# Kernel optimization log

Hardware: AMD Instinct MI355X
Metric: run time of the kernel (lower is better)

The kernel has to match this reference:

```python
import jax, jax.numpy as jnp
import numpy as np

B, N, C, S, G, COOR = 4, 8192, 64, 2048, 32, 3
C2 = 2 * C            # channels after SetAbstraction
EXP = 4
RADII = (0.2, 0.4, 0.4)


def _sqdist(src, dst):
    # (B,M,3),(B,N,3) -> (B,M,N) squared distances (same expansion as torch code)
    d = -2.0 * jnp.einsum('bmc,bnc->bmn', src, dst)
    d = d + jnp.sum(src ** 2, -1)[:, :, None]
    d = d + jnp.sum(dst ** 2, -1)[:, None, :]
    return d


def _gather(points, idx):
    # points (B,N,C), idx (B,...) -> (B,...,C)
    return jax.vmap(lambda p, i: p[i])(points, idx)


def _fps(xyz, npoint):
    # xyz (B,N,3) -> (B,npoint) farthest point sample indices (start at index 0)
    b, n, _ = xyz.shape

    def step(carry, _):
        distance, farthest = carry
        centroid = jnp.take_along_axis(xyz, farthest[:, None, None], axis=1)  # (B,1,3)
        d = jnp.sqrt(jnp.sum((xyz - centroid) ** 2, -1))
        distance = jnp.minimum(distance, d)
        nxt = jnp.argmax(distance, -1)
        return (distance, nxt), farthest

    init = (jnp.full((b, n), 1e10, xyz.dtype), jnp.zeros((b,), jnp.int32))
    _, idxs = jax.lax.scan(step, init, None, length=npoint)
    return jnp.transpose(idxs)  # (B,npoint)


def _query_hybrid(radius, nsample, xyz, new_xyz):
    d = _sqdist(new_xyz, xyz)                       # (B,S,N)
    neg_d, idx = jax.lax.top_k(-d, nsample)         # smallest distances
    mask = (-neg_d) > radius ** 2
    first = idx[:, :, :1]
    return jnp.where(mask, first, idx)              # (B,S,nsample)


def _group(coor, new_coor, fea, radius, nsample):
    # coor (B,N,3), new_coor (B,S,3), fea (B,N,C) -> (B,S,G,C+3)
    gi = _query_hybrid(radius, nsample, coor, new_coor)
    gc = (_gather(coor, gi) - new_coor[:, :, None, :]) / radius
    gf = _gather(fea, gi)
    return jnp.concatenate([gf, gc], axis=-1)


def _mlp_max(g, w):
    # g (B,S,G,Cin), w (Cout,Cin): 1x1 conv (no bias) + ReLU, then max over group
    h = jax.nn.relu(jnp.einsum('bsgc,dc->bsgd', g, w))
    return jnp.max(h, axis=2)  # (B,S,Cout)


def _inv_res_mlp(coor, fea, radius, nsample, w_la, w1, w2):
    # coor (B,S,3), fea (B,S,C2) channels-last
    identity = fea
    g = _group(coor, coor, fea, radius, nsample)
    fea = _mlp_max(g, w_la)                              # LocalAggregation
    fea = jax.nn.relu(jnp.einsum('bsc,dc->bsd', fea, w1))
    fea = jnp.einsum('bsc,dc->bsd', fea, w2)             # last ReLU dropped
    return jax.nn.relu(fea + identity)


def setup_inputs() -> dict:
    key = jax.random.key(0)
    ks = jax.random.split(key, 10)
    def w(k, o, i):
        return jax.random.normal(k, (o, i), jnp.float32) / np.sqrt(i)
    return {
        'points_coor': jax.random.uniform(ks[0], (B, 3, N), jnp.float32),
        'points_fea': jax.random.normal(ks[1], (B, C, N), jnp.float32),
        'w_sa':  w(ks[2], C2, C + COOR),
        'w_la1': w(ks[3], C2, C2 + COOR),
        'w1_1':  w(ks[4], C2 * EXP, C2),
        'w2_1':  w(ks[5], C2, C2 * EXP),
        'w_la2': w(ks[6], C2, C2 + COOR),
        'w1_2':  w(ks[7], C2 * EXP, C2),
        'w2_2':  w(ks[8], C2, C2 * EXP),
    }


def reference(points_coor, points_fea, w_sa, w_la1, w1_1, w2_1, w_la2, w1_2, w2_2):
    coor = jnp.transpose(points_coor, (0, 2, 1))  # (B,N,3)
    fea = jnp.transpose(points_fea, (0, 2, 1))    # (B,N,C)
    # SetAbstraction: S-G-P
    fps_idx = _fps(coor, S)
    new_coor = _gather(coor, fps_idx)             # (B,S,3)
    g = _group(coor, new_coor, fea, RADII[0], G)
    new_fea = _mlp_max(g, w_sa)                   # (B,S,2C)
    # InvResMLP blocks
    new_fea = _inv_res_mlp(new_coor, new_fea, RADII[1], G, w_la1, w1_1, w2_1)
    new_fea = _inv_res_mlp(new_coor, new_fea, RADII[2], G, w_la2, w1_2, w2_2)
    return (jnp.transpose(new_coor, (0, 2, 1)), jnp.transpose(new_fea, (0, 2, 1)))
```

## Files before the change

### kernel.cpp

```cpp
#include <hip/hip_runtime.h>
#include <hip/hip_bf16.h>

#define BB 4
#define NN 8192
#define CC 64
#define SS 2048
#define GG 32
#define C2V 128
#define HHV 512

typedef unsigned long long u64;
typedef unsigned int u32;

__global__ void k_transpose_fea(const float* __restrict__ in, float* __restrict__ out) {
  __shared__ float tile[32][33];
  const int b = blockIdx.z;
  const int n0 = blockIdx.x * 32, c0 = blockIdx.y * 32;
  const int tx = threadIdx.x, ty = threadIdx.y;
  const float* src = in + (size_t)b * CC * NN;
#pragma unroll
  for (int i = 0; i < 32; i += 8)
    tile[ty + i][tx] = src[(size_t)(c0 + ty + i) * NN + n0 + tx];
  __syncthreads();
  float* dst = out + (size_t)b * NN * CC;
#pragma unroll
  for (int i = 0; i < 32; i += 8)
    dst[(size_t)(n0 + ty + i) * CC + c0 + tx] = tile[tx][ty + i];
}

__global__ __launch_bounds__(1024, 4) void k_fps(const float* __restrict__ pc, int* __restrict__ fps_idx) {
#pragma clang fp contract(off)
  __shared__ float lx[NN], ly[NN], lz[NN];
  __shared__ int sIdx[SS];
  __shared__ u64 sK[2][16];
  const int b = blockIdx.x, tid = threadIdx.x;
  const int lane = tid & 63, wid = tid >> 6;
  const float* pb = pc + (size_t)b * 3 * NN;
  {
    const float4* gx = (const float4*)pb;
    const float4* gy = (const float4*)(pb + NN);
    const float4* gz = (const float4*)(pb + 2 * NN);
    float4* sx = (float4*)lx; float4* sy = (float4*)ly; float4* sz = (float4*)lz;
    sx[tid] = gx[tid]; sx[tid + 1024] = gx[tid + 1024];
    sy[tid] = gy[tid]; sy[tid + 1024] = gy[tid + 1024];
    sz[tid] = gz[tid]; sz[tid + 1024] = gz[tid + 1024];
  }
  if (tid < 32) ((u64*)sK)[tid] = 0ull;
  if (tid == 0) sK[0][0] = ~0ull;
  __syncthreads();

  const int fbase = wid * 64 + lane;
  const u32 ibase = (u32)(wid * 256 + lane * 4);
  float4 D0 = make_float4(1e20f, 1e20f, 1e20f, 1e20f);
  float4 D1 = D0;

#define DPPK64(K, CTL) { \
      u32 lo = (u32)(K), hi = (u32)((K) >> 32); \
      u32 lo2 = (u32)__builtin_amdgcn_update_dpp(0, (int)lo, CTL, 0xf, 0xf, false); \
      u32 hi2 = (u32)__builtin_amdgcn_update_dpp(0, (int)hi, CTL, 0xf, 0xf, false); \
      u64 k2 = ((u64)hi2 << 32) | (u64)lo2; if (k2 > (K)) (K) = k2; }
#define RMAXF(V, CTL) { \
      float t_ = __int_as_float(__builtin_amdgcn_update_dpp(0, __float_as_int(V), CTL, 0xf, 0xf, false)); \
      (V) = fmaxf((V), t_); }
#define RMINU(V, CTL) { \
      u32 t_ = (u32)__builtin_amdgcn_update_dpp(0, (int)(V), CTL, 0xf, 0xf, false); \
      (V) = min((V), t_); }

  for (int k = 0; k < SS; ++k) {
    const int p = k & 1, pn = p ^ 1;
    u64 kk = sK[p][lane & 15];
    const float4 Xa = ((const float4*)lx)[fbase], Xb = ((const float4*)lx)[fbase + 1024];
    const float4 Ya = ((const float4*)ly)[fbase], Yb = ((const float4*)ly)[fbase + 1024];
    const float4 Za = ((const float4*)lz)[fbase], Zb = ((const float4*)lz)[fbase + 1024];
    DPPK64(kk, 0x121) DPPK64(kk, 0x122) DPPK64(kk, 0x124) DPPK64(kk, 0x128)
    const u32 idx = 0xFFFFFFFFu - (u32)kk;
    if (tid == 0) sIdx[k] = (int)idx;
    const float cx = lx[idx], cy = ly[idx], cz = lz[idx];

#define UPDC(XX, YY, ZZ, DD) { \
      float dx_ = (XX) - cx, dy_ = (YY) - cy, dz_ = (ZZ) - cz; \
      float t0_ = dx_ * dx_, t1_ = dy_ * dy_, t2_ = dz_ * dz_; \
      float s_ = (t0_ + t1_) + t2_; \
      (DD) = fminf((DD), s_); }
    UPDC(Xa.x, Ya.x, Za.x, D0.x) UPDC(Xa.y, Ya.y, Za.y, D0.y)
    UPDC(Xa.z, Ya.z, Za.z, D0.z) UPDC(Xa.w, Ya.w, Za.w, D0.w)
    UPDC(Xb.x, Yb.x, Zb.x, D1.x) UPDC(Xb.y, Yb.y, Zb.y, D1.y)
    UPDC(Xb.z, Yb.z, Zb.z, D1.z) UPDC(Xb.w, Yb.w, Zb.w, D1.w)
#undef UPDC

    float m2 = fmaxf(fmaxf(fmaxf(D0.x, D0.y), fmaxf(D0.z, D0.w)),
                     fmaxf(fmaxf(D1.x, D1.y), fmaxf(D1.z, D1.w)));
    RMAXF(m2, 0x121) RMAXF(m2, 0x122) RMAXF(m2, 0x124) RMAXF(m2, 0x128)
    m2 = fmaxf(m2, __shfl_xor(m2, 16, 64));
    m2 = fmaxf(m2, __shfl_xor(m2, 32, 64));

    float s = sqrtf(m2);
    u32 sbits = __float_as_uint(s);
    float spred = __uint_as_float(sbits - 1u);
    double M = ((double)spred + (double)s) * 0.5;
    double L = M * M;
    if (sbits & 1u) L = __longlong_as_double(__double_as_longlong(L) + 1ll);
    float Lf = (float)L;
    if ((double)Lf < L) Lf = __uint_as_float(__float_as_uint(Lf) + 1u);

    u32 enc = 0xFFFFFFFFu;
    {
      int off = -1;
      if (D1.w >= Lf) off = 4096 + 3;
      if (D1.z >= Lf) off = 4096 + 2;
      if (D1.y >= Lf) off = 4096 + 1;
      if (D1.x >= Lf) off = 4096 + 0;
      if (D0.w >= Lf) off = 3;
      if (D0.z >= Lf) off = 2;
      if (D0.y >= Lf) off = 1;
      if (D0.x >= Lf) off = 0;
      if (off >= 0) enc = ibase + (u32)off;
    }
    RMINU(enc, 0x121) RMINU(enc, 0x122) RMINU(enc, 0x124) RMINU(enc, 0x128)
    enc = min(enc, (u32)__shfl_xor((int)enc, 16, 64));
    enc = min(enc, (u32)__shfl_xor((int)enc, 32, 64));

    if (lane == 0)
      sK[pn][wid] = (((u64)sbits) << 32) | (u64)(0xFFFFFFFFu - enc);
    __syncthreads();
  }
#undef DPPK64
#undef RMAXF
#undef RMINU
  fps_idx[b * SS + tid] = sIdx[tid];
  fps_idx[b * SS + 1024 + tid] = sIdx[1024 + tid];
}

__global__ void k_gather(const float* __restrict__ pc, const int* __restrict__ fps_idx,
                         float* __restrict__ ncoor, float* __restrict__ out0) {
  int t = blockIdx.x * 256 + threadIdx.x;
  if (t >= BB * SS) return;
  int b = t / SS, s = t % SS;
  int id = fps_idx[t];
  const float* base = pc + (size_t)b * 3 * NN;
  float x = base[id], y = base[NN + id], z = base[2 * NN + id];
  ncoor[(size_t)t * 3] = x; ncoor[(size_t)t * 3 + 1] = y; ncoor[(size_t)t * 3 + 2] = z;
  size_t o = (size_t)b * 3 * SS + s;
  out0[o] = x; out0[o + SS] = y; out0[o + 2 * SS] = z;
}

__global__ __launch_bounds__(256) void k_knn(const float* __restrict__ candp,
                                             const float* __restrict__ newc,
                                             int mode, int ncand, float r2,
                                             int* __restrict__ gidx) {
  __shared__ float cd[2048];
  __shared__ int ci[2048];
  __shared__ int hist[64];
  __shared__ int cnt, oc, binT, mlow;
  const int q = blockIdx.x, tid = threadIdx.x;
  const int b = q / SS;
  if (tid == 0) { cnt = 0; oc = 0; }
  if (tid < 64) hist[tid] = 0;
  __syncthreads();
  const float qx = newc[(size_t)q * 3], qy = newc[(size_t)q * 3 + 1], qz = newc[(size_t)q * 3 + 2];
  float qn;
  {
#pragma clang fp contract(off)
    qn = (qx * qx + qy * qy) + qz * qz;
  }
  const float sc = 64.0f / r2;
  const float* base = (mode == 0) ? candp + (size_t)b * 3 * NN : candp + (size_t)b * SS * 3;
  for (int i = tid; i < ncand; i += 256) {
    float x, y, z;
    if (mode == 0) { x = base[i]; y = base[NN + i]; z = base[2 * NN + i]; }
    else { x = base[3 * i]; y = base[3 * i + 1]; z = base[3 * i + 2]; }
    float dot = fmaf(qz, z, fmaf(qy, y, qx * x));
    float d;
    {
#pragma clang fp contract(off)
      float pn = (x * x + y * y) + z * z;
      d = ((-2.0f * dot) + qn) + pn;
    }
    if (d <= r2) {
      int pp = atomicAdd(&cnt, 1);
      if (pp < 2048) { cd[pp] = d; ci[pp] = i; }
      float db = (d > 0.0f) ? d : 0.0f;
      atomicAdd(&hist[min(63, (int)(db * sc))], 1);
    }
  }
  __syncthreads();
  const int M = min(cnt, 2048);
  if (tid == 0) {
    if (M > 32) {
      int c = 0, t = 0;
      for (t = 0; t < 64; ++t) { if (c + hist[t] >= 32) break; c += hist[t]; }
      binT = t; mlow = c;
    } else binT = -1;
  }
  __syncthreads();
  int* out = gidx + (size_t)q * 32;
  if (binT < 0) {
    for (int j = tid; j < M; j += 256) out[atomicAdd(&oc, 1)] = ci[j];
    __syncthreads();
    if (tid == 0 && M < 32) {
      float bd = 1e30f; int bx = 0x7FFFFFFF;
      for (int j = 0; j < M; ++j)
        if (cd[j] < bd || (cd[j] == bd && ci[j] < bx)) { bd = cd[j]; bx = ci[j]; }
      for (int j = M; j < 32; ++j) out[j] = bx;
    }
  } else {
    const int bt = binT, m = mlow;
    for (int j = tid; j < M; j += 256) {
      float dbj = (cd[j] > 0.0f) ? cd[j] : 0.0f;
      int bin = min(63, (int)(dbj * sc));
      if (bin < bt) out[atomicAdd(&oc, 1)] = ci[j];
      else if (bin == bt) {
        int r = 0; const float dj = cd[j]; const int ij = ci[j];
        for (int kk = 0; kk < M; ++kk) {
          float dbk = (cd[kk] > 0.0f) ? cd[kk] : 0.0f;
          if (min(63, (int)(dbk * sc)) == bt &&
              (cd[kk] < dj || (cd[kk] == dj && ci[kk] < ij))) ++r;
        }
        if (m + r < 32) out[m + r] = ci[j];
      }
    }
  }
}

template <int FDIM>
__global__ __launch_bounds__(256) void k_group_mlp(
    const float* __restrict__ fea, const int* __restrict__ gidx,
    const float* __restrict__ newc, const float* __restrict__ candp,
    int mode, int ncand, float radius,
    const float* __restrict__ wp, float* __restrict__ outf) {
  constexpr int CP4 = FDIM + 4;
  constexpr int NC4 = CP4 / 4;
  __shared__ float4 g4[2][32][NC4];
  __shared__ int sidx[2][32];
  __shared__ float sq[2][3];
  __shared__ float pf[2][4][128];
  const int tid = threadIdx.x;
  const int rs = tid >> 7, tl = tid & 127;
  const int dt = tl & 31, et = tl >> 5;
  const int d0 = dt * 4, e0 = et * 8;
  const int row0 = blockIdx.x * 16;
  for (int rp = 0; rp < 16; rp += 2) {
    const int row = row0 + rp + rs;
    if (tl < 32) sidx[rs][tl] = gidx[(size_t)row * 32 + tl];
    if (tl < 3) sq[rs][tl] = newc[(size_t)row * 3 + tl];
    __syncthreads();
    const int bb2 = row / SS;
    const float* fb = fea + (size_t)bb2 * ncand * FDIM;
    const float* cb = (mode == 0) ? candp + (size_t)bb2 * 3 * NN
                                  : candp + (size_t)bb2 * SS * 3;
    float* gf = (float*)&g4[rs][0][0];
    for (int qq = tl; qq < 32 * CP4; qq += 128) {
      int e = qq / CP4, c = qq - e * CP4;
      int id = sidx[rs][e];
      float v;
      if (c < FDIM) v = fb[(size_t)id * FDIM + c];
      else if (c < FDIM + 3) {
        int comp = c - FDIM;
        float pcv = (mode == 0) ? cb[(size_t)comp * NN + id] : cb[(size_t)id * 3 + comp];
        v = (pcv - sq[rs][comp]) / radius;
      } else v = 0.0f;
      gf[qq] = v;
    }
    __syncthreads();
    float acc[4][8];
#pragma unroll
    for (int i = 0; i < 4; ++i)
#pragma unroll
      for (int j = 0; j < 8; ++j) acc[i][j] = 0.0f;
    const float4* w4 = (const float4*)wp;
    for (int c4 = 0; c4 < NC4; ++c4) {
      float4 wv[4], gv[8];
#pragma unroll
      for (int i = 0; i < 4; ++i) wv[i] = w4[(size_t)(d0 + i) * NC4 + c4];
#pragma unroll
      for (int j = 0; j < 8; ++j) gv[j] = g4[rs][e0 + j][c4];
#pragma unroll
      for (int i = 0; i < 4; ++i)
#pragma unroll
        for (int j = 0; j < 8; ++j) {
          acc[i][j] += wv[i].x * gv[j].x;
          acc[i][j] += wv[i].y * gv[j].y;
          acc[i][j] += wv[i].z * gv[j].z;
          acc[i][j] += wv[i].w * gv[j].w;
        }
    }
#pragma unroll
    for (int i = 0; i < 4; ++i) {
      float m = acc[i][0];
#pragma unroll
      for (int j = 1; j < 8; ++j) m = fmaxf(m, acc[i][j]);
      pf[rs][et][d0 + i] = m;
    }
    __syncthreads();
    {
      const int d = tid & 127, r2s = tid >> 7;
      const int rowW = row0 + rp + r2s;
      float m = fmaxf(fmaxf(pf[r2s][0][d], pf[r2s][1][d]),
                      fmaxf(pf[r2s][2][d], pf[r2s][3][d]));
      outf[(size_t)rowW * 128 + d] = fmaxf(m, 0.0f);
    }
    __syncthreads();
  }
}

template <bool RESID>
__global__ __launch_bounds__(256) void k_dense(
    const float* __restrict__ A, const float* __restrict__ W,
    const float* __restrict__ Id, float* __restrict__ Out,
    int K, int Ntot) {
  __shared__ float4 sa[64][17], sb[64][17];
  const int m0 = blockIdx.x * 64, n0 = blockIdx.y * 64;
  const int tid = threadIdx.x;
  const int mt = tid & 15, nt = tid >> 4;
  float acc[4][4];
#pragma unroll
  for (int i = 0; i < 4; ++i)
#pragma unroll
    for (int j = 0; j < 4; ++j) acc[i][j] = 0.0f;
  for (int kc = 0; kc < K; kc += 64) {
    for (int q2 = tid; q2 < 2048; q2 += 256) {
      int half = q2 >> 10, qq = q2 & 1023;
      int r = qq >> 4, c = qq & 15;
      const float* src = half ? (W + (size_t)(n0 + r) * K + kc + c * 4)
                              : (A + (size_t)(m0 + r) * K + kc + c * 4);
      float4 v = *(const float4*)src;
      if (half) sb[r][c] = v; else sa[r][c] = v;
    }
    __syncthreads();
#pragma unroll
    for (int c = 0; c < 16; ++c) {
      const int ks = (c + mt + nt) & 15;
      float4 av[4], bv[4];
#pragma unroll
      for (int i = 0; i < 4; ++i) av[i] = sa[mt * 4 + i][ks];
#pragma unroll
      for (int j = 0; j < 4; ++j) bv[j] = sb[nt * 4 + j][ks];
#pragma unroll
      for (int i = 0; i < 4; ++i)
#pragma unroll
        for (int j = 0; j < 4; ++j) {
          acc[i][j] += av[i].x * bv[j].x;
          acc[i][j] += av[i].y * bv[j].y;
          acc[i][j] += av[i].z * bv[j].z;
          acc[i][j] += av[i].w * bv[j].w;
        }
    }
    __syncthreads();
  }
#pragma unroll
  for (int i = 0; i < 4; ++i)
#pragma unroll
    for (int j = 0; j < 4; ++j) {
      size_t o = (size_t)(m0 + mt * 4 + i) * Ntot + n0 + nt * 4 + j;
      float v = acc[i][j];
      if (RESID) v += Id[o];
      Out[o] = fmaxf(v, 0.0f);
    }
}

__global__ void k_pad_w(const float* __restrict__ src, float* __restrict__ dst,
                        int rows, int cin, int cp4) {
  int t = blockIdx.x * 256 + threadIdx.x;
  if (t >= rows * cp4) return;
  int r = t / cp4, c = t - r * cp4;
  dst[t] = (c < cin) ? src[(size_t)r * cin + c] : 0.0f;
}

__global__ void k_out1_t(const float* __restrict__ in, float* __restrict__ out) {
  __shared__ float tile[32][33];
  const int b = blockIdx.z;
  const int s0 = blockIdx.x * 32, d0 = blockIdx.y * 32;
  const int tx = threadIdx.x, ty = threadIdx.y;
#pragma unroll
  for (int i = 0; i < 32; i += 8)
    tile[ty + i][tx] = in[(size_t)(b * SS + s0 + ty + i) * 128 + d0 + tx];
  __syncthreads();
#pragma unroll
  for (int i = 0; i < 32; i += 8)
    out[(size_t)(b * 128 + d0 + ty + i) * SS + s0 + tx] = tile[tx][ty + i];
}

extern "C" void kernel_launch(void* const* d_in, const int* in_sizes, int n_in,
                              void* d_out, int out_size, void* d_ws, size_t ws_size,
                              hipStream_t stream) {
  const float* pc    = (const float*)d_in[0];
  const float* pfea  = (const float*)d_in[1];
  const float* w_sa  = (const float*)d_in[2];
  const float* w_la1 = (const float*)d_in[3];
  const float* w1_1  = (const float*)d_in[4];
  const float* w2_1  = (const float*)d_in[5];
  const float* w_la2 = (const float*)d_in[6];
  const float* w1_2  = (const float*)d_in[7];
  const float* w2_2  = (const float*)d_in[8];
  float* out0 = (float*)d_out;
  float* out1 = out0 + (size_t)BB * 3 * SS;

  char* wsp = (char*)d_ws;
  size_t off = 0;
  auto alloc = [&](size_t bytes) -> void* {
    void* p = wsp + off;
    off = (off + bytes + 255) & ~(size_t)255;
    return p;
  };
  float* hbuf = (float*)alloc((size_t)BB * SS * HHV * 4);
  float* feaT = hbuf;
  int*   fpsi = (int*)alloc((size_t)BB * SS * 4);
  float* ncoor = (float*)alloc((size_t)BB * SS * 3 * 4);
  int*   gi = (int*)alloc((size_t)BB * SS * GG * 4);
  float* fa = (float*)alloc((size_t)BB * SS * C2V * 4);
  float* fb = (float*)alloc((size_t)BB * SS * C2V * 4);
  float* wsap = (float*)alloc(128 * 68 * 4);
  float* wla1p = (float*)alloc(128 * 132 * 4);
  float* wla2p = (float*)alloc(128 * 132 * 4);

  k_pad_w<<<dim3((128 * 68 + 255) / 256), dim3(256), 0, stream>>>(w_sa, wsap, 128, 67, 68);
  k_pad_w<<<dim3((128 * 132 + 255) / 256), dim3(256), 0, stream>>>(w_la1, wla1p, 128, 131, 132);
  k_pad_w<<<dim3((128 * 132 + 255) / 256), dim3(256), 0, stream>>>(w_la2, wla2p, 128, 131, 132);

  k_transpose_fea<<<dim3(NN / 32, CC / 32, BB), dim3(32, 8), 0, stream>>>(pfea, feaT);
  k_fps<<<dim3(BB), dim3(1024), 0, stream>>>(pc, fpsi);
  k_gather<<<dim3((BB * SS + 255) / 256), dim3(256), 0, stream>>>(pc, fpsi, ncoor, out0);

  k_knn<<<dim3(BB * SS), dim3(256), 0, stream>>>(pc, ncoor, 0, NN, 0.04f, gi);
  k_group_mlp<64><<<dim3(BB * SS / 16), dim3(256), 0, stream>>>(feaT, gi, ncoor, pc, 0, NN, 0.2f, wsap, fa);

  k_knn<<<dim3(BB * SS), dim3(256), 0, stream>>>(ncoor, ncoor, 1, SS, 0.16f, gi);

  k_group_mlp<128><<<dim3(BB * SS / 16), dim3(256), 0, stream>>>(fa, gi, ncoor, ncoor, 1, SS, 0.4f, wla1p, fb);
  k_dense<false><<<dim3(128, 8), dim3(256), 0, stream>>>(fb, w1_1, nullptr, hbuf, 128, 512);
  k_dense<true><<<dim3(128, 2), dim3(256), 0, stream>>>(hbuf, w2_1, fa, fb, 512, 128);

  k_group_mlp<128><<<dim3(BB * SS / 16), dim3(256), 0, stream>>>(fb, gi, ncoor, ncoor, 1, SS, 0.4f, wla2p, fa);
  k_dense<false><<<dim3(128, 8), dim3(256), 0, stream>>>(fa, w1_2, nullptr, hbuf, 128, 512);
  k_dense<true><<<dim3(128, 2), dim3(256), 0, stream>>>(hbuf, w2_2, fb, fa, 512, 128);

  k_out1_t<<<dim3(SS / 32, 128 / 32, BB), dim3(32, 8), 0, stream>>>(fa, out1);
}
```

Before: 4.281 ms.

## Shrink FPS block to 512 threads with AGPR-parked coordinates; spread group MLP rows

```diff
diff --git a/kernel.cpp b/kernel.cpp
--- a/kernel.cpp
+++ b/kernel.cpp
@@ -28,31 +28,54 @@
     dst[(size_t)(n0 + ty + i) * CC + c0 + tx] = tile[tx][ty + i];
 }
 
-__global__ __launch_bounds__(1024, 4) void k_fps(const float* __restrict__ pc, int* __restrict__ fps_idx) {
+__global__ __launch_bounds__(512, 2) void k_fps(const float* __restrict__ pc, int* __restrict__ fps_idx) {
 #pragma clang fp contract(off)
   __shared__ float lx[NN], ly[NN], lz[NN];
   __shared__ int sIdx[SS];
-  __shared__ u64 sK[2][16];
+  __shared__ u64 sK[2][8];
   const int b = blockIdx.x, tid = threadIdx.x;
   const int lane = tid & 63, wid = tid >> 6;
   const float* pb = pc + (size_t)b * 3 * NN;
+
+  const float4* gx = (const float4*)pb;
+  const float4* gy = (const float4*)(pb + NN);
+  const float4* gz = (const float4*)(pb + 2 * NN);
+  float4 vX0 = gx[tid * 4 + 0], vX1 = gx[tid * 4 + 1], vX2 = gx[tid * 4 + 2], vX3 = gx[tid * 4 + 3];
+  float4 vY0 = gy[tid * 4 + 0], vY1 = gy[tid * 4 + 1], vY2 = gy[tid * 4 + 2], vY3 = gy[tid * 4 + 3];
+  float4 vZ0 = gz[tid * 4 + 0], vZ1 = gz[tid * 4 + 1], vZ2 = gz[tid * 4 + 2], vZ3 = gz[tid * 4 + 3];
   {
-    const float4* gx = (const float4*)pb;
-    const float4* gy = (const float4*)(pb + NN);
-    const float4* gz = (const float4*)(pb + 2 * NN);
     float4* sx = (float4*)lx; float4* sy = (float4*)ly; float4* sz = (float4*)lz;
-    sx[tid] = gx[tid]; sx[tid + 1024] = gx[tid + 1024];
-    sy[tid] = gy[tid]; sy[tid + 1024] = gy[tid + 1024];
-    sz[tid] = gz[tid]; sz[tid + 1024] = gz[tid + 1024];
-  }
-  if (tid < 32) ((u64*)sK)[tid] = 0ull;
+    sx[tid * 4 + 0] = vX0; sx[tid * 4 + 1] = vX1; sx[tid * 4 + 2] = vX2; sx[tid * 4 + 3] = vX3;
+    sy[tid * 4 + 0] = vY0; sy[tid * 4 + 1] = vY1; sy[tid * 4 + 2] = vY2; sy[tid * 4 + 3] = vY3;
+    sz[tid * 4 + 0] = vZ0; sz[tid * 4 + 1] = vZ1; sz[tid * 4 + 2] = vZ2; sz[tid * 4 + 3] = vZ3;
+  }
+  float aX0x, aX0y, aX0z, aX0w, aX1x, aX1y, aX1z, aX1w;
+  float aX2x, aX2y, aX2z, aX2w, aX3x, aX3y, aX3z, aX3w;
+  float aY0x, aY0y, aY0z, aY0w, aY1x, aY1y, aY1z, aY1w;
+  float aY2x, aY2y, aY2z, aY2w, aY3x, aY3y, aY3z, aY3w;
+  float aZ0x, aZ0y, aZ0z, aZ0w, aZ1x, aZ1y, aZ1z, aZ1w;
+  float aZ2x, aZ2y, aZ2z, aZ2w, aZ3x, aZ3y, aZ3z, aZ3w;
+#define PARK(A, V) asm volatile("v_accvgpr_write_b32 %0, %1" : "=a"(A) : "v"(V));
+  PARK(aX0x, vX0.x) PARK(aX0y, vX0.y) PARK(aX0z, vX0.z) PARK(aX0w, vX0.w)
+  PARK(aX1x, vX1.x) PARK(aX1y, vX1.y) PARK(aX1z, vX1.z) PARK(aX1w, vX1.w)
+  PARK(aX2x, vX2.x) PARK(aX2y, vX2.y) PARK(aX2z, vX2.z) PARK(aX2w, vX2.w)
+  PARK(aX3x, vX3.x) PARK(aX3y, vX3.y) PARK(aX3z, vX3.z) PARK(aX3w, vX3.w)
+  PARK(aY0x, vY0.x) PARK(aY0y, vY0.y) PARK(aY0z, vY0.z) PARK(aY0w, vY0.w)
+  PARK(aY1x, vY1.x) PARK(aY1y, vY1.y) PARK(aY1z, vY1.z) PARK(aY1w, vY1.w)
+  PARK(aY2x, vY2.x) PARK(aY2y, vY2.y) PARK(aY2z, vY2.z) PARK(aY2w, vY2.w)
+  PARK(aY3x, vY3.x) PARK(aY3y, vY3.y) PARK(aY3z, vY3.z) PARK(aY3w, vY3.w)
+  PARK(aZ0x, vZ0.x) PARK(aZ0y, vZ0.y) PARK(aZ0z, vZ0.z) PARK(aZ0w, vZ0.w)
+  PARK(aZ1x, vZ1.x) PARK(aZ1y, vZ1.y) PARK(aZ1z, vZ1.z) PARK(aZ1w, vZ1.w)
+  PARK(aZ2x, vZ2.x) PARK(aZ2y, vZ2.y) PARK(aZ2z, vZ2.z) PARK(aZ2w, vZ2.w)
+  PARK(aZ3x, vZ3.x) PARK(aZ3y, vZ3.y) PARK(aZ3z, vZ3.z) PARK(aZ3w, vZ3.w)
+#undef PARK
+  if (lane == 0) sK[0][wid] = 0ull;
   if (tid == 0) sK[0][0] = ~0ull;
   __syncthreads();
 
-  const int fbase = wid * 64 + lane;
-  const u32 ibase = (u32)(wid * 256 + lane * 4);
+  const u32 ibase = (u32)(tid * 16);
   float4 D0 = make_float4(1e20f, 1e20f, 1e20f, 1e20f);
-  float4 D1 = D0;
+  float4 D1 = D0, D2q = D0, D3 = D0;
 
 #define DPPK64(K, CTL) { \
       u32 lo = (u32)(K), hi = (u32)((K) >> 32); \
@@ -65,14 +88,30 @@
 #define RMINU(V, CTL) { \
       u32 t_ = (u32)__builtin_amdgcn_update_dpp(0, (int)(V), CTL, 0xf, 0xf, false); \
       (V) = min((V), t_); }
+#define FETCH(V, A) asm volatile("v_accvgpr_read_b32 %0, %1" : "=v"(V) : "a"(A));
 
   for (int k = 0; k < SS; ++k) {
     const int p = k & 1, pn = p ^ 1;
-    u64 kk = sK[p][lane & 15];
-    const float4 Xa = ((const float4*)lx)[fbase], Xb = ((const float4*)lx)[fbase + 1024];
-    const float4 Ya = ((const float4*)ly)[fbase], Yb = ((const float4*)ly)[fbase + 1024];
-    const float4 Za = ((const float4*)lz)[fbase], Zb = ((const float4*)lz)[fbase + 1024];
-    DPPK64(kk, 0x121) DPPK64(kk, 0x122) DPPK64(kk, 0x124) DPPK64(kk, 0x128)
+    u64 kk = sK[p][lane & 7];
+    float x0x, x0y, x0z, x0w, x1x, x1y, x1z, x1w;
+    float x2x, x2y, x2z, x2w, x3x, x3y, x3z, x3w;
+    float y0x, y0y, y0z, y0w, y1x, y1y, y1z, y1w;
+    float y2x, y2y, y2z, y2w, y3x, y3y, y3z, y3w;
+    float z0x, z0y, z0z, z0w, z1x, z1y, z1z, z1w;
+    float z2x, z2y, z2z, z2w, z3x, z3y, z3z, z3w;
+    FETCH(x0x, aX0x) FETCH(x0y, aX0y) FETCH(x0z, aX0z) FETCH(x0w, aX0w)
+    FETCH(x1x, aX1x) FETCH(x1y, aX1y) FETCH(x1z, aX1z) FETCH(x1w, aX1w)
+    FETCH(x2x, aX2x) FETCH(x2y, aX2y) FETCH(x2z, aX2z) FETCH(x2w, aX2w)
+    FETCH(x3x, aX3x) FETCH(x3y, aX3y) FETCH(x3z, aX3z) FETCH(x3w, aX3w)
+    FETCH(y0x, aY0x) FETCH(y0y, aY0y) FETCH(y0z, aY0z) FETCH(y0w, aY0w)
+    FETCH(y1x, aY1x) FETCH(y1y, aY1y) FETCH(y1z, aY1z) FETCH(y1w, aY1w)
+    FETCH(y2x, aY2x) FETCH(y2y, aY2y) FETCH(y2z, aY2z) FETCH(y2w, aY2w)
+    FETCH(y3x, aY3x) FETCH(y3y, aY3y) FETCH(y3z, aY3z) FETCH(y3w, aY3w)
+    FETCH(z0x, aZ0x) FETCH(z0y, aZ0y) FETCH(z0z, aZ0z) FETCH(z0w, aZ0w)
+    FETCH(z1x, aZ1x) FETCH(z1y, aZ1y) FETCH(z1z, aZ1z) FETCH(z1w, aZ1w)
+    FETCH(z2x, aZ2x) FETCH(z2y, aZ2y) FETCH(z2z, aZ2z) FETCH(z2w, aZ2w)
+    FETCH(z3x, aZ3x) FETCH(z3y, aZ3y) FETCH(z3z, aZ3z) FETCH(z3w, aZ3w)
+    DPPK64(kk, 0x121) DPPK64(kk, 0x122) DPPK64(kk, 0x124)
     const u32 idx = 0xFFFFFFFFu - (u32)kk;
     if (tid == 0) sIdx[k] = (int)idx;
     const float cx = lx[idx], cy = ly[idx], cz = lz[idx];
@@ -82,14 +121,21 @@
       float t0_ = dx_ * dx_, t1_ = dy_ * dy_, t2_ = dz_ * dz_; \
       float s_ = (t0_ + t1_) + t2_; \
       (DD) = fminf((DD), s_); }
-    UPDC(Xa.x, Ya.x, Za.x, D0.x) UPDC(Xa.y, Ya.y, Za.y, D0.y)
-    UPDC(Xa.z, Ya.z, Za.z, D0.z) UPDC(Xa.w, Ya.w, Za.w, D0.w)
-    UPDC(Xb.x, Yb.x, Zb.x, D1.x) UPDC(Xb.y, Yb.y, Zb.y, D1.y)
-    UPDC(Xb.z, Yb.z, Zb.z, D1.z) UPDC(Xb.w, Yb.w, Zb.w, D1.w)
+    UPDC(x0x, y0x, z0x, D0.x) UPDC(x0y, y0y, z0y, D0.y)
+    UPDC(x0z, y0z, z0z, D0.z) UPDC(x0w, y0w, z0w, D0.w)
+    UPDC(x1x, y1x, z1x, D1.x) UPDC(x1y, y1y, z1y, D1.y)
+    UPDC(x1z, y1z, z1z, D1.z) UPDC(x1w, y1w, z1w, D1.w)
+    UPDC(x2x, y2x, z2x, D2q.x) UPDC(x2y, y2y, z2y, D2q.y)
+    UPDC(x2z, y2z, z2z, D2q.z) UPDC(x2w, y2w, z2w, D2q.w)
+    UPDC(x3x, y3x, z3x, D3.x) UPDC(x3y, y3y, z3y, D3.y)
+    UPDC(x3z, y3z, z3z, D3.z) UPDC(x3w, y3w, z3w, D3.w)
 #undef UPDC
 
-    float m2 = fmaxf(fmaxf(fmaxf(D0.x, D0.y), fmaxf(D0.z, D0.w)),
-                     fmaxf(fmaxf(D1.x, D1.y), fmaxf(D1.z, D1.w)));
+    float m2 = fmaxf(
+        fmaxf(fmaxf(fmaxf(D0.x, D0.y), fmaxf(D0.z, D0.w)),
+              fmaxf(fmaxf(D1.x, D1.y), fmaxf(D1.z, D1.w))),
+        fmaxf(fmaxf(fmaxf(D2q.x, D2q.y), fmaxf(D2q.z, D2q.w)),
+              fmaxf(fmaxf(D3.x, D3.y), fmaxf(D3.z, D3.w))));
     RMAXF(m2, 0x121) RMAXF(m2, 0x122) RMAXF(m2, 0x124) RMAXF(m2, 0x128)
     m2 = fmaxf(m2, __shfl_xor(m2, 16, 64));
     m2 = fmaxf(m2, __shfl_xor(m2, 32, 64));
@@ -106,10 +152,18 @@
     u32 enc = 0xFFFFFFFFu;
     {
       int off = -1;
-      if (D1.w >= Lf) off = 4096 + 3;
-      if (D1.z >= Lf) off = 4096 + 2;
-      if (D1.y >= Lf) off = 4096 + 1;
-      if (D1.x >= Lf) off = 4096 + 0;
+      if (D3.w >= Lf) off = 15;
+      if (D3.z >= Lf) off = 14;
+      if (D3.y >= Lf) off = 13;
+      if (D3.x >= Lf) off = 12;
+      if (D2q.w >= Lf) off = 11;
+      if (D2q.z >= Lf) off = 10;
+      if (D2q.y >= Lf) off = 9;
+      if (D2q.x >= Lf) off = 8;
+      if (D1.w >= Lf) off = 7;
+      if (D1.z >= Lf) off = 6;
+      if (D1.y >= Lf) off = 5;
+      if (D1.x >= Lf) off = 4;
       if (D0.w >= Lf) off = 3;
       if (D0.z >= Lf) off = 2;
       if (D0.y >= Lf) off = 1;
@@ -127,8 +181,10 @@
 #undef DPPK64
 #undef RMAXF
 #undef RMINU
-  fps_idx[b * SS + tid] = sIdx[tid];
-  fps_idx[b * SS + 1024 + tid] = sIdx[1024 + tid];
+#undef FETCH
+#pragma unroll
+  for (int q = 0; q < 4; ++q)
+    fps_idx[b * SS + q * 512 + tid] = sIdx[q * 512 + tid];
 }
 
 __global__ void k_gather(const float* __restrict__ pc, const int* __restrict__ fps_idx,
@@ -238,8 +294,8 @@
   const int rs = tid >> 7, tl = tid & 127;
   const int dt = tl & 31, et = tl >> 5;
   const int d0 = dt * 4, e0 = et * 8;
-  const int row0 = blockIdx.x * 16;
-  for (int rp = 0; rp < 16; rp += 2) {
+  const int row0 = blockIdx.x * 4;
+  for (int rp = 0; rp < 4; rp += 2) {
     const int row = row0 + rp + rs;
     if (tl < 32) sidx[rs][tl] = gidx[(size_t)row * 32 + tl];
     if (tl < 3) sq[rs][tl] = newc[(size_t)row * 3 + tl];
@@ -418,19 +474,19 @@
   k_pad_w<<<dim3((128 * 132 + 255) / 256), dim3(256), 0, stream>>>(w_la2, wla2p, 128, 131, 132);
 
   k_transpose_fea<<<dim3(NN / 32, CC / 32, BB), dim3(32, 8), 0, stream>>>(pfea, feaT);
-  k_fps<<<dim3(BB), dim3(1024), 0, stream>>>(pc, fpsi);
+  k_fps<<<dim3(BB), dim3(512), 0, stream>>>(pc, fpsi);
   k_gather<<<dim3((BB * SS + 255) / 256), dim3(256), 0, stream>>>(pc, fpsi, ncoor, out0);
 
   k_knn<<<dim3(BB * SS), dim3(256), 0, stream>>>(pc, ncoor, 0, NN, 0.04f, gi);
-  k_group_mlp<64><<<dim3(BB * SS / 16), dim3(256), 0, stream>>>(feaT, gi, ncoor, pc, 0, NN, 0.2f, wsap, fa);
+  k_group_mlp<64><<<dim3(BB * SS / 4), dim3(256), 0, stream>>>(feaT, gi, ncoor, pc, 0, NN, 0.2f, wsap, fa);
 
   k_knn<<<dim3(BB * SS), dim3(256), 0, stream>>>(ncoor, ncoor, 1, SS, 0.16f, gi);
 
-  k_group_mlp<128><<<dim3(BB * SS / 16), dim3(256), 0, stream>>>(fa, gi, ncoor, ncoor, 1, SS, 0.4f, wla1p, fb);
+  k_group_mlp<128><<<dim3(BB * SS / 4), dim3(256), 0, stream>>>(fa, gi, ncoor, ncoor, 1, SS, 0.4f, wla1p, fb);
   k_dense<false><<<dim3(128, 8), dim3(256), 0, stream>>>(fb, w1_1, nullptr, hbuf, 128, 512);
   k_dense<true><<<dim3(128, 2), dim3(256), 0, stream>>>(hbuf, w2_1, fa, fb, 512, 128);
 
-  k_group_mlp<128><<<dim3(BB * SS / 16), dim3(256), 0, stream>>>(fb, gi, ncoor, ncoor, 1, SS, 0.4f, wla2p, fa);
+  k_group_mlp<128><<<dim3(BB * SS / 4), dim3(256), 0, stream>>>(fb, gi, ncoor, ncoor, 1, SS, 0.4f, wla2p, fa);
   k_dense<false><<<dim3(128, 8), dim3(256), 0, stream>>>(fa, w1_2, nullptr, hbuf, 128, 512);
   k_dense<true><<<dim3(128, 2), dim3(256), 0, stream>>>(hbuf, w2_2, fb, fa, 512, 128);
 
```

Measured after the change: 3.717 ms, median of 2. 1.15x faster.
